# Performance work log

Hardware: AMD Instinct MI355X
Metric: run time of the kernel (lower is better)

Reference implementation:

```python
import jax, jax.numpy as jnp
import numpy as np

N = 50000      # nodes
E = 800000     # edges (avg degree 16)
IN = 128       # in_channels
H = 128        # hidden_channels
K = 20         # n_clusters
ALPHA = 0.2


def _glorot(key, shape):
    lim = float(np.sqrt(6.0 / (shape[0] + shape[1])))
    return jax.random.uniform(key, shape, jnp.float32, -lim, lim)


def setup_inputs() -> dict:
    key = jax.random.key(0)
    ks = jax.random.split(key, 12)
    x = jax.random.normal(ks[0], (N, IN), jnp.float32)
    edge_index = jax.random.randint(ks[1], (2, E), 0, N, dtype=jnp.int64)
    edge_weight = jax.random.uniform(ks[2], (E,), jnp.float32)
    perm = jax.random.permutation(ks[3], N).astype(jnp.int64)
    W1 = _glorot(ks[4], (IN, H)); b1 = jnp.zeros((H,), jnp.float32)
    W2 = _glorot(ks[5], (H, H));  b2 = jnp.zeros((H,), jnp.float32)
    W3 = _glorot(ks[6], (H, H));  b3 = jnp.zeros((H,), jnp.float32)
    W4 = _glorot(ks[7], (H, H));  b4 = jnp.zeros((H,), jnp.float32)
    prelu_a = jnp.full((H,), 0.25, jnp.float32)
    Wc = _glorot(ks[8], (H, IN)); bc = jnp.zeros((IN,), jnp.float32)
    mu = jax.random.normal(ks[9], (K, IN), jnp.float32)
    return dict(x=x, edge_index=edge_index, edge_weight=edge_weight, perm=perm,
                W1=W1, b1=b1, W2=W2, b2=b2, W3=W3, b3=b3, W4=W4, b4=b4,
                prelu_a=prelu_a, Wc=Wc, bc=bc, mu=mu)


def _gcn_norm(src, dst, ew, n):
    # add self-loops (weight 1) + symmetric normalization, PyG gcn_norm
    loop = jnp.arange(n)
    src2 = jnp.concatenate([src, loop])
    dst2 = jnp.concatenate([dst, loop])
    w2 = jnp.concatenate([ew, jnp.ones((n,), ew.dtype)])
    deg = jax.ops.segment_sum(w2, dst2, num_segments=n)
    dinv = jnp.where(deg > 0, jax.lax.rsqrt(deg), 0.0)
    norm = dinv[src2] * w2 * dinv[dst2]
    return src2, dst2, norm


def _gcn_conv(x, W, b, src2, dst2, norm, n):
    h = x @ W                              # [n, out]
    msg = h[src2] * norm[:, None]          # gather + scale
    return jax.ops.segment_sum(msg, dst2, num_segments=n) + b


def reference(x, edge_index, edge_weight, perm, W1, b1, W2, b2, W3, b3, W4, b4,
              prelu_a, Wc, bc, mu):
    n = x.shape[0]
    src, dst = edge_index[0], edge_index[1]
    src2, dst2, norm = _gcn_norm(src, dst, edge_weight, n)

    def encoder(h):
        h = _gcn_conv(h, W1, b1, src2, dst2, norm, n)
        h = _gcn_conv(h, W2, b2, src2, dst2, norm, n)
        h = _gcn_conv(h, W3, b3, src2, dst2, norm, n)
        h = _gcn_conv(h, W4, b4, src2, dst2, norm, n)
        return jnp.where(h >= 0, h, prelu_a * h)  # PReLU

    pos_z = encoder(x)
    neg_z = encoder(x[perm])                       # corruption: permute node rows
    summary = jax.nn.sigmoid(pos_z.mean(axis=0))   # [H]

    x_out = _gcn_conv(pos_z, Wc, bc, src2, dst2, norm, n)  # [N, IN]

    # Student's-t soft assignment: ||x_i - mu_k||^2 via expansion (same math)
    d = (jnp.sum(x_out * x_out, axis=1, keepdims=True)
         + jnp.sum(mu * mu, axis=1)[None, :]
         - 2.0 * (x_out @ mu.T))
    d = jnp.maximum(d, 0.0)
    q = 1.0 / (1.0 + d / ALPHA + 1e-8)
    q = q ** (ALPHA + 1.0) / 2.0
    q = q / jnp.sum(q, axis=1, keepdims=True)
    return pos_z, neg_z, summary, x_out, q
```

## Files before the change

kernel.cpp:

```cpp
#include <hip/hip_runtime.h>
#include <hip/hip_bf16.h>

constexpr int NN = 50000;
constexpr int EE = 800000;
constexpr int C  = 128;
constexpr int KC = 20;
constexpr int NB = (NN + 1023) / 1024;

typedef __attribute__((ext_vector_type(8))) short bf16x8;
typedef __attribute__((ext_vector_type(4))) float f32x4;
typedef __attribute__((ext_vector_type(4))) unsigned int u32x4;
typedef unsigned long long u64;

__device__ inline unsigned short f2bf(float f) {
    unsigned u = __float_as_uint(f);
    u += 0x7fff + ((u >> 16) & 1);
    return (unsigned short)(u >> 16);
}
__device__ inline float bf2f(unsigned short h) {
    return __uint_as_float(((unsigned)h) << 16);
}


__global__ __launch_bounds__(256) void k_scan1(const unsigned* __restrict__ cnt,
                                               unsigned* __restrict__ bsum) {
    __shared__ unsigned red[256];
    int b = blockIdx.x, t = threadIdx.x;
    int i0 = b * 1024 + t * 4;
    unsigned s = 0;
    #pragma unroll
    for (int j = 0; j < 4; ++j) { int i = i0 + j; s += (i < NN) ? cnt[i] : 0u; }
    red[t] = s; __syncthreads();
    for (int st = 128; st > 0; st >>= 1) { if (t < st) red[t] += red[t + st]; __syncthreads(); }
    if (t == 0) bsum[b] = red[0];
}

__global__ void k_scan2(unsigned* bsum, unsigned* total) {
    int t = threadIdx.x;
    unsigned v = (t < NB) ? bsum[t] : 0u;
    unsigned x = v;
    #pragma unroll
    for (int s = 1; s < 64; s <<= 1) { unsigned u = __shfl_up(x, s, 64); if (t >= s) x += u; }
    if (t < NB) bsum[t] = x - v;
    if (t == 63) *total = x;
}

__global__ __launch_bounds__(256) void k_scan3(const unsigned* __restrict__ cnt,
                                               const unsigned* __restrict__ bsum,
                                               const unsigned* __restrict__ total,
                                               unsigned* __restrict__ off,
                                               unsigned* __restrict__ cursor) {
    __shared__ unsigned wred[4];
    int b = blockIdx.x, t = threadIdx.x, lane = t & 63, wv = t >> 6;
    int i0 = b * 1024 + t * 4;
    unsigned v[4]; unsigned s = 0;
    #pragma unroll
    for (int j = 0; j < 4; ++j) { int i = i0 + j; v[j] = (i < NN) ? cnt[i] : 0u; s += v[j]; }
    unsigned x = s;
    #pragma unroll
    for (int st = 1; st < 64; st <<= 1) { unsigned u = __shfl_up(x, st, 64); if (lane >= st) x += u; }
    if (lane == 63) wred[wv] = x;
    __syncthreads();
    unsigned woff = 0;
    for (int k = 0; k < 4; ++k) if (k < wv) woff += wred[k];
    unsigned excl = bsum[b] + woff + x - s;
    #pragma unroll
    for (int j = 0; j < 4; ++j) {
        int i = i0 + j;
        if (i < NN) { off[i] = excl; cursor[i] = excl; excl += v[j]; }
    }
    if (b == 0 && t == 0) off[NN] = *total;
}

__global__ void k_fill(const int* __restrict__ ei, const float* __restrict__ ew,
                       unsigned* cursor, uint2* __restrict__ em) {
    int e = blockIdx.x * 256 + threadIdx.x;
    if (e >= EE) return;
    int s = __builtin_nontemporal_load(ei + e);
    int d = __builtin_nontemporal_load(ei + EE + e);
    float ww = __builtin_nontemporal_load(ew + e);
    unsigned p = atomicAdd(&cursor[d], 1u);
    u64 v = (u64)__float_as_uint(ww) << 32 | (unsigned)s;
    __builtin_nontemporal_store(v, (u64*)(em + p));
}

__global__ void k_dinv_csr(const unsigned* __restrict__ off,
                           const uint2* __restrict__ em, float* __restrict__ dinv) {
    int i = blockIdx.x * 256 + threadIdx.x;
    if (i >= NN) return;
    unsigned p0 = off[i], p1 = off[i + 1];
    float s = 1.0f;
    for (unsigned p = p0; p < p1; ++p) s += __uint_as_float(em[p].y);
    dinv[i] = (s > 0.f) ? rsqrtf(s) : 0.f;
}

__global__ void k_scale(const unsigned* __restrict__ off, const float* __restrict__ dinv,
                        uint2* __restrict__ em) {
    int i = blockIdx.x * 256 + threadIdx.x;
    if (i >= NN) return;
    float di = dinv[i];
    unsigned p0 = off[i], p1 = off[i + 1];
    for (unsigned p = p0; p < p1; ++p) {
        uint2 e = em[p];
        em[p].y = __float_as_uint(dinv[e.x] * __uint_as_float(e.y) * di);
    }
}


__global__ void k_wsplit(const float* W0, const float* W1, const float* W2,
                         const float* W3, const float* W4,
                         unsigned short* __restrict__ wt) {
    int m = blockIdx.x >> 6;
    const float* W = (m == 0) ? W0 : (m == 1) ? W1 : (m == 2) ? W2 : (m == 3) ? W3 : W4;
    int idx = (blockIdx.x & 63) * 256 + threadIdx.x;
    int k = idx >> 7, j = idx & 127;
    float v = W[idx];
    unsigned short h = f2bf(v);
    unsigned short* hi = wt + (size_t)(2 * m) * C * C;
    unsigned short* lo = wt + (size_t)(2 * m + 1) * C * C;
    hi[j * C + k] = h;
    lo[j * C + k] = f2bf(v - bf2f(h));
}


__global__ __launch_bounds__(256) void k_hist_mm(const int* __restrict__ ei,
                                                 unsigned* cnt,
                                                 const float* __restrict__ A,
                                                 const unsigned short* __restrict__ Bh,
                                                 const unsigned short* __restrict__ Bl,
                                                 unsigned short* __restrict__ G,
                                                 int histBlocks) {
    int tid = threadIdx.x;
    if (blockIdx.x < histBlocks) {
        int e = blockIdx.x * 256 + tid;
        if (e < EE) atomicAdd(&cnt[__builtin_nontemporal_load(ei + EE + e)], 1u);
        return;
    }
    __shared__ unsigned short Ah[64 * 128];
    __shared__ unsigned short Al[64 * 128];
    int lane = tid & 63;
    int wv   = tid >> 6;
    int row0 = (blockIdx.x - histBlocks) * 64;

    {
        int r  = tid >> 2;
        int c0 = (tid & 3) * 32;
        int gr = row0 + r;
        bool ok = gr < NN;
        const float* src = A + (size_t)(ok ? gr : 0) * C + c0;
        #pragma unroll
        for (int g = 0; g < 4; ++g) {
            float f[8];
            if (ok) {
                *(float4*)&f[0] = *(const float4*)(src + g * 8);
                *(float4*)&f[4] = *(const float4*)(src + g * 8 + 4);
            } else {
                #pragma unroll
                for (int j = 0; j < 8; ++j) f[j] = 0.f;
            }
            union { unsigned short u[8]; uint4 v; } ph, pl;
            #pragma unroll
            for (int j = 0; j < 8; ++j) {
                unsigned short h = f2bf(f[j]);
                ph.u[j] = h;
                pl.u[j] = f2bf(f[j] - bf2f(h));
            }
            int k = c0 + g * 8;
            int byte = (r * 256 + k * 2) ^ ((r & 7) << 4);
            *(uint4*)((char*)Ah + byte) = ph.v;
            *(uint4*)((char*)Al + byte) = pl.v;
        }
    }

    bf16x8 bh[2][4], bl[2][4];
    #pragma unroll
    for (int cf = 0; cf < 2; ++cf) {
        int col = wv * 32 + cf * 16 + (lane & 15);
        #pragma unroll
        for (int kt = 0; kt < 4; ++kt) {
            int k = kt * 32 + (lane >> 4) * 8;
            bh[cf][kt] = *(const bf16x8*)(Bh + (size_t)col * C + k);
            bl[cf][kt] = *(const bf16x8*)(Bl + (size_t)col * C + k);
        }
    }

    __syncthreads();

    f32x4 zero = {0.f, 0.f, 0.f, 0.f};
    f32x4 acc[4][2];
    #pragma unroll
    for (int rf = 0; rf < 4; ++rf)
        #pragma unroll
        for (int cf = 0; cf < 2; ++cf) acc[rf][cf] = zero;

    #pragma unroll
    for (int rf = 0; rf < 4; ++rf) {
        int row = rf * 16 + (lane & 15);
        #pragma unroll
        for (int kt = 0; kt < 4; ++kt) {
            int k = kt * 32 + (lane >> 4) * 8;
            int byte = (row * 256 + k * 2) ^ ((row & 7) << 4);
            bf16x8 ah = *(const bf16x8*)((const char*)Ah + byte);
            bf16x8 al = *(const bf16x8*)((const char*)Al + byte);
            #pragma unroll
            for (int cf = 0; cf < 2; ++cf) {
                acc[rf][cf] = __builtin_amdgcn_mfma_f32_16x16x32_bf16(ah, bh[cf][kt], acc[rf][cf], 0, 0, 0);
                acc[rf][cf] = __builtin_amdgcn_mfma_f32_16x16x32_bf16(al, bh[cf][kt], acc[rf][cf], 0, 0, 0);
                acc[rf][cf] = __builtin_amdgcn_mfma_f32_16x16x32_bf16(ah, bl[cf][kt], acc[rf][cf], 0, 0, 0);
            }
        }
    }

    #pragma unroll
    for (int cf = 0; cf < 2; ++cf) {
        int col = wv * 32 + cf * 16 + (lane & 15);
        #pragma unroll
        for (int rf = 0; rf < 4; ++rf) {
            #pragma unroll
            for (int q = 0; q < 4; ++q) {
                int row = row0 + rf * 16 + (lane >> 4) * 4 + q;
                if (row < NN) G[(size_t)row * C + col] = f2bf(acc[rf][cf][q]);
            }
        }
    }
}


__global__ __launch_bounds__(256) void k_mm2(const unsigned short* __restrict__ Ap,
                                             const unsigned short* __restrict__ An,
                                             const unsigned short* __restrict__ Bh,
                                             const unsigned short* __restrict__ Bl,
                                             unsigned short* __restrict__ Gp,
                                             unsigned short* __restrict__ Gn, int nblk) {
    __shared__ unsigned short Ah[64 * 128];
    int tid  = threadIdx.x;
    int lane = tid & 63;
    int wv   = tid >> 6;
    int chain = blockIdx.x >= nblk;
    int blk   = chain ? blockIdx.x - nblk : blockIdx.x;
    const unsigned short* A = chain ? An : Ap;
    unsigned short*       G = chain ? Gn : Gp;
    int row0 = blk * 64;

    {
        int r  = tid >> 2;
        int c0 = (tid & 3) * 32;
        int gr = row0 + r;
        bool ok = gr < NN;
        const unsigned short* s = A + (size_t)(ok ? gr : 0) * C + c0;
        #pragma unroll
        for (int g = 0; g < 4; ++g) {
            uint4 v = ok ? *(const uint4*)(s + g * 8) : make_uint4(0, 0, 0, 0);
            int k = c0 + g * 8;
            int byte = (r * 256 + k * 2) ^ ((r & 7) << 4);
            *(uint4*)((char*)Ah + byte) = v;
        }
    }

    bf16x8 bh[2][4], bl[2][4];
    #pragma unroll
    for (int cf = 0; cf < 2; ++cf) {
        int col = wv * 32 + cf * 16 + (lane & 15);
        #pragma unroll
        for (int kt = 0; kt < 4; ++kt) {
            int k = kt * 32 + (lane >> 4) * 8;
            bh[cf][kt] = *(const bf16x8*)(Bh + (size_t)col * C + k);
            bl[cf][kt] = *(const bf16x8*)(Bl + (size_t)col * C + k);
        }
    }

    __syncthreads();

    f32x4 zero = {0.f, 0.f, 0.f, 0.f};
    f32x4 acc[4][2];
    #pragma unroll
    for (int rf = 0; rf < 4; ++rf)
        #pragma unroll
        for (int cf = 0; cf < 2; ++cf) acc[rf][cf] = zero;

    #pragma unroll
    for (int rf = 0; rf < 4; ++rf) {
        int row = rf * 16 + (lane & 15);
        #pragma unroll
        for (int kt = 0; kt < 4; ++kt) {
            int k = kt * 32 + (lane >> 4) * 8;
            int byte = (row * 256 + k * 2) ^ ((row & 7) << 4);
            bf16x8 a = *(const bf16x8*)((const char*)Ah + byte);
            #pragma unroll
            for (int cf = 0; cf < 2; ++cf) {
                acc[rf][cf] = __builtin_amdgcn_mfma_f32_16x16x32_bf16(a, bh[cf][kt], acc[rf][cf], 0, 0, 0);
                acc[rf][cf] = __builtin_amdgcn_mfma_f32_16x16x32_bf16(a, bl[cf][kt], acc[rf][cf], 0, 0, 0);
            }
        }
    }

    #pragma unroll
    for (int cf = 0; cf < 2; ++cf) {
        int col = wv * 32 + cf * 16 + (lane & 15);
        #pragma unroll
        for (int rf = 0; rf < 4; ++rf) {
            #pragma unroll
            for (int q = 0; q < 4; ++q) {
                int row = row0 + rf * 16 + (lane >> 4) * 4 + q;
                if (row < NN) G[(size_t)row * C + col] = f2bf(acc[rf][cf][q]);
            }
        }
    }
}


__global__ __launch_bounds__(256) void k_agg2(const unsigned short* __restrict__ Gp,
                                              const unsigned short* __restrict__ Gn,
                                              const int* __restrict__ permN,
                                              const float* __restrict__ dinv,
                                              const unsigned* __restrict__ off,
                                              const uint2* __restrict__ em,
                                              const float* __restrict__ bias,
                                              const float* __restrict__ prelu,
                                              unsigned short* planeP, unsigned short* planeN,
                                              float* fP, float* fN, int nb) {
    __shared__ uint2 sem[4][64];
    int tid   = threadIdx.x;
    int chain = blockIdx.x >= nb;
    int blk   = chain ? blockIdx.x - nb : blockIdx.x;
    int lane  = tid & 63;
    int wid   = tid >> 6;
    int half  = lane >> 5;
    int gg    = (lane >> 4) & 1;
    int il    = lane & 15;
    int l32   = lane & 31;
    int i     = (blk * 4 + wid) * 2 + half;
    bool act  = i < NN;
    const unsigned short* Gsel = chain ? Gn : Gp;
    const int*            prm  = chain ? permN : nullptr;
    const uint4* H4 = (const uint4*)Gsel;

    float a[8];
    {
        int si = act ? (prm ? prm[i] : i) : 0;
        uint4 hv = H4[(size_t)si * 16 + il];
        float dv = act ? dinv[i] : 0.f;
        float sn = (gg == 0) ? dv * dv : 0.f;
        a[0] = __uint_as_float(hv.x << 16) * sn;
        a[1] = __uint_as_float(hv.x & 0xffff0000u) * sn;
        a[2] = __uint_as_float(hv.y << 16) * sn;
        a[3] = __uint_as_float(hv.y & 0xffff0000u) * sn;
        a[4] = __uint_as_float(hv.z << 16) * sn;
        a[5] = __uint_as_float(hv.z & 0xffff0000u) * sn;
        a[6] = __uint_as_float(hv.w << 16) * sn;
        a[7] = __uint_as_float(hv.w & 0xffff0000u) * sn;
    }

    unsigned p0 = 0, p1 = 0;
    if (act) { p0 = off[i]; p1 = off[i + 1]; }
    for (unsigned base = p0; base < p1; base += 32) {
        unsigned rem = p1 - base;
        int cap = rem < 32u ? (int)rem : 32;
        u64 ev = __builtin_nontemporal_load(
            (const u64*)(em + base + ((unsigned)l32 < rem ? (unsigned)l32 : 0u)));
        sem[wid][half * 32 + l32] = make_uint2((unsigned)ev, (unsigned)(ev >> 32));
        #pragma unroll 4
        for (int t = gg; t < cap; t += 2) {
            uint2 e = sem[wid][half * 32 + t];
            unsigned sv = e.x;
            if (prm) sv = (unsigned)prm[sv];
            float wv = __uint_as_float(e.y);
            uint4 hv = H4[(size_t)sv * 16 + il];
            a[0] += __uint_as_float(hv.x << 16) * wv;
            a[1] += __uint_as_float(hv.x & 0xffff0000u) * wv;
            a[2] += __uint_as_float(hv.y << 16) * wv;
            a[3] += __uint_as_float(hv.y & 0xffff0000u) * wv;
            a[4] += __uint_as_float(hv.z << 16) * wv;
            a[5] += __uint_as_float(hv.z & 0xffff0000u) * wv;
            a[6] += __uint_as_float(hv.w << 16) * wv;
            a[7] += __uint_as_float(hv.w & 0xffff0000u) * wv;
        }
    }

    #pragma unroll
    for (int j = 0; j < 8; ++j)
        a[j] += __shfl_xor(a[j], 16, 64);

    {
        float bv[8];
        *(float4*)&bv[0] = *(const float4*)(bias + il * 8);
        *(float4*)&bv[4] = *(const float4*)(bias + il * 8 + 4);
        #pragma unroll
        for (int j = 0; j < 8; ++j) a[j] += bv[j];
        if (prelu) {
            float pv[8];
            *(float4*)&pv[0] = *(const float4*)(prelu + il * 8);
            *(float4*)&pv[4] = *(const float4*)(prelu + il * 8 + 4);
            #pragma unroll
            for (int j = 0; j < 8; ++j) a[j] = (a[j] >= 0.f) ? a[j] : pv[j] * a[j];
        }
    }

    unsigned short* plane = chain ? planeN : planeP;
    float*          fo    = chain ? fN : fP;
    if (act) {
        if (gg == 0 && plane) {
            u32x4 o = { (unsigned)f2bf(a[0]) | ((unsigned)f2bf(a[1]) << 16),
                        (unsigned)f2bf(a[2]) | ((unsigned)f2bf(a[3]) << 16),
                        (unsigned)f2bf(a[4]) | ((unsigned)f2bf(a[5]) << 16),
                        (unsigned)f2bf(a[6]) | ((unsigned)f2bf(a[7]) << 16) };
            __builtin_nontemporal_store(o, (u32x4*)((uint4*)plane + (size_t)i * 16 + il));
        }
        if (fo) {
            f32x4 v0 = { a[0], a[1], a[2], a[3] };
            f32x4 v1 = { a[4], a[5], a[6], a[7] };
            if (gg == 0) __builtin_nontemporal_store(v0, (f32x4*)(fo + (size_t)i * C + il * 8));
            else         __builtin_nontemporal_store(v1, (f32x4*)(fo + (size_t)i * C + il * 8 + 4));
        }
    }
}


__global__ __launch_bounds__(256) void k_sum(const float* __restrict__ pos, float* sumbuf) {
    __shared__ float red[256];
    int t = threadIdx.x;
    int c = t & 127;
    int half = t >> 7;
    float acc = 0.f;
    for (int r = blockIdx.x * 2 + half; r < NN; r += gridDim.x * 2)
        acc += pos[(size_t)r * C + c];
    red[t] = acc;
    __syncthreads();
    if (half == 0) atomicAdd(&sumbuf[c], acc + red[t + 128]);
}

__global__ void k_summary(const float* sumbuf, float* out) {
    int t = threadIdx.x;
    if (t < C) {
        float m = sumbuf[t] * (1.0f / (float)NN);
        out[t] = 1.0f / (1.0f + expf(-m));
    }
}


__global__ __launch_bounds__(256) void k_q(const float* __restrict__ xo,
                                           const float* __restrict__ mu,
                                           float* __restrict__ qout) {
    __shared__ float sx[64][132];
    __shared__ float smu[KC][128];
    __shared__ float smun[KC];
    int tid = threadIdx.x;
    for (int idx = tid; idx < KC * 128; idx += 256)
        smu[idx >> 7][idx & 127] = mu[idx];
    __syncthreads();
    if (tid < KC) {
        float s = 0.f;
        #pragma unroll 4
        for (int j = 0; j < 128; ++j) { float m = smu[tid][j]; s += m * m; }
        smun[tid] = s;
    }
    int n0 = blockIdx.x * 64;
    for (int idx = tid; idx < 64 * 32; idx += 256) {
        int r = idx >> 5;
        int c = (idx & 31) * 4;
        int gr = n0 + r;
        float4 v = make_float4(0.f, 0.f, 0.f, 0.f);
        if (gr < NN) v = *(const float4*)(xo + (size_t)gr * C + c);
        *(float4*)&sx[r][c] = v;
    }
    __syncthreads();
    int lr = tid >> 2;
    int g  = tid & 3;
    int node = n0 + lr;
    if (node < NN) {
        float ss = 0.f;
        #pragma unroll 8
        for (int j = 0; j < 128; ++j) { float x = sx[lr][j]; ss += x * x; }
        float qv[5]; float qs = 0.f;
        #pragma unroll
        for (int kk = 0; kk < 5; ++kk) {
            int k = g * 5 + kk;
            float dot = 0.f;
            #pragma unroll 8
            for (int j = 0; j < 128; ++j) dot += sx[lr][j] * smu[k][j];
            float d = ss + smun[k] - 2.0f * dot;
            d = fmaxf(d, 0.f);
            float q = 1.0f / (1.0f + d * 5.0f + 1e-8f);
            q = powf(q, 1.2f) * 0.5f;
            qv[kk] = q; qs += q;
        }
        qs += __shfl_xor(qs, 1, 64);
        qs += __shfl_xor(qs, 2, 64);
        float inv = 1.0f / qs;
        #pragma unroll
        for (int kk = 0; kk < 5; ++kk)
            qout[(size_t)node * KC + g * 5 + kk] = qv[kk] * inv;
    }
}


extern "C" void kernel_launch(void* const* d_in, const int* in_sizes, int n_in,
                              void* d_out, int out_size, void* d_ws, size_t ws_size,
                              hipStream_t stream) {
    const float* x    = (const float*)d_in[0];
    const int*   ei   = (const int*)d_in[1];
    const float* ew   = (const float*)d_in[2];
    const int*   perm = (const int*)d_in[3];
    const float* W1 = (const float*)d_in[4];  const float* b1 = (const float*)d_in[5];
    const float* W2 = (const float*)d_in[6];  const float* b2 = (const float*)d_in[7];
    const float* W3 = (const float*)d_in[8];  const float* b3 = (const float*)d_in[9];
    const float* W4 = (const float*)d_in[10]; const float* b4 = (const float*)d_in[11];
    const float* prelu_a = (const float*)d_in[12];
    const float* Wc = (const float*)d_in[13]; const float* bc = (const float*)d_in[14];
    const float* mu = (const float*)d_in[15];

    float* out     = (float*)d_out;
    float* pos_z   = out;
    float* neg_z   = out + (size_t)NN * C;
    float* summary = out + (size_t)2 * NN * C;
    float* xout    = summary + C;
    float* qout    = xout + (size_t)NN * C;

    char* w = (char*)d_ws;
    auto carve = [&](size_t bytes) { void* p = (void*)w; w += (bytes + 511) & ~(size_t)511; return p; };
    float*          dinv   = (float*)carve((size_t)NN * 4);
    unsigned*       cnt    = (unsigned*)carve((size_t)(NN + 1) * 4);
    unsigned*       cursor = (unsigned*)carve((size_t)NN * 4);
    unsigned*       bsum   = (unsigned*)carve(256 * 4);
    unsigned*       total  = (unsigned*)carve(64);
    uint2*          em     = (uint2*)carve((size_t)EE * 8);
    float*          sumbuf = (float*)carve(512);
    unsigned short* wt     = (unsigned short*)carve((size_t)5 * 2 * C * C * 2);
    unsigned short* Gp     = (unsigned short*)carve((size_t)NN * C * 2);
    unsigned short* Gn     = (unsigned short*)carve((size_t)NN * C * 2);
    unsigned short* P0     = (unsigned short*)carve((size_t)NN * C * 2);
    unsigned short* P1     = (unsigned short*)carve((size_t)NN * C * 2);
    unsigned short* P2     = (unsigned short*)carve((size_t)NN * C * 2);

    unsigned short* Wh[5], *Wl[5];
    for (int m = 0; m < 5; ++m) {
        Wh[m] = wt + (size_t)(2 * m) * C * C;
        Wl[m] = wt + (size_t)(2 * m + 1) * C * C;
    }

    hipMemsetAsync(cnt, 0, (size_t)(NN + 1) * 4, stream);
    hipMemsetAsync(sumbuf, 0, 512, stream);

    int gE = (EE + 255) / 256, gN = (NN + 255) / 256;
    int gM = (NN + 63) / 64;
    int gA = (NN + 7) / 8;

    k_wsplit<<<320, 256, 0, stream>>>(W1, W2, W3, W4, Wc, wt);

    k_hist_mm<<<gE + gM, 256, 0, stream>>>(ei, cnt, x, Wh[0], Wl[0], Gp, gE);

    k_scan1<<<NB, 256, 0, stream>>>(cnt, bsum);
    k_scan2<<<1, 64, 0, stream>>>(bsum, total);
    k_scan3<<<NB, 256, 0, stream>>>(cnt, bsum, total, cnt, cursor);
    k_fill <<<gE, 256, 0, stream>>>(ei, ew, cursor, em);
    k_dinv_csr<<<gN, 256, 0, stream>>>(cnt, em, dinv);
    k_scale<<<gN, 256, 0, stream>>>(cnt, dinv, em);

    k_agg2<<<2 * gA, 256, 0, stream>>>(Gp, Gp, perm, dinv, cnt, em, b1, nullptr,
                                       P0, P1, nullptr, nullptr, gA);
    k_mm2 <<<2 * gM, 256, 0, stream>>>(P0, P1, Wh[1], Wl[1], Gp, Gn, gM);
    k_agg2<<<2 * gA, 256, 0, stream>>>(Gp, Gn, nullptr, dinv, cnt, em, b2, nullptr,
                                       P0, P1, nullptr, nullptr, gA);
    k_mm2 <<<2 * gM, 256, 0, stream>>>(P0, P1, Wh[2], Wl[2], Gp, Gn, gM);
    k_agg2<<<2 * gA, 256, 0, stream>>>(Gp, Gn, nullptr, dinv, cnt, em, b3, nullptr,
                                       P0, P1, nullptr, nullptr, gA);
    k_mm2 <<<2 * gM, 256, 0, stream>>>(P0, P1, Wh[3], Wl[3], Gp, Gn, gM);
    k_agg2<<<2 * gA, 256, 0, stream>>>(Gp, Gn, nullptr, dinv, cnt, em, b4, prelu_a,
                                       P2, nullptr, pos_z, neg_z, gA);
    k_mm2 <<<gM, 256, 0, stream>>>(P2, P2, Wh[4], Wl[4], Gp, Gn, gM);
    k_agg2<<<gA, 256, 0, stream>>>(Gp, Gp, nullptr, dinv, cnt, em, bc, nullptr,
                                   nullptr, nullptr, xout, nullptr, gA);

    k_sum<<<256, 256, 0, stream>>>(pos_z, sumbuf);
    k_summary<<<1, 128, 0, stream>>>(sumbuf, summary);

    k_q<<<(NN + 63) / 64, 256, 0, stream>>>(xout, mu, qout);
}
```

Baseline: 593.5 us.

## Fuse positive and negative chain aggregation into one kernel sharing edge reads

The aggregation kernel now processes the positive and corrupted chains together for the same destination node. Each CSR edge entry is loaded once and used for two gathers, instead of two separate blocks each reading the edge list. A templated flag removes the permutation lookup when it is not needed, and a specialised single-chain kernel handles the final output layer. The cost is twice the accumulator registers per thread, which may lower occupancy, and the edge-fill store is switched from nontemporal to a normal store.

```diff
diff --git a/kernel.cpp b/kernel.cpp
--- a/kernel.cpp
+++ b/kernel.cpp
@@ -80,8 +80,7 @@
     int d = __builtin_nontemporal_load(ei + EE + e);
     float ww = __builtin_nontemporal_load(ew + e);
     unsigned p = atomicAdd(&cursor[d], 1u);
-    u64 v = (u64)__float_as_uint(ww) << 32 | (unsigned)s;
-    __builtin_nontemporal_store(v, (u64*)(em + p));
+    em[p] = make_uint2((unsigned)s, __float_as_uint(ww));
 }
 
 __global__ void k_dinv_csr(const unsigned* __restrict__ off,
@@ -309,46 +308,55 @@
 }
 
 
-__global__ __launch_bounds__(256) void k_agg2(const unsigned short* __restrict__ Gp,
+template<bool PERMN>
+__global__ __launch_bounds__(256) void k_agg3(const unsigned short* __restrict__ Gp,
                                               const unsigned short* __restrict__ Gn,
-                                              const int* __restrict__ permN,
+                                              const int* __restrict__ perm,
                                               const float* __restrict__ dinv,
                                               const unsigned* __restrict__ off,
                                               const uint2* __restrict__ em,
                                               const float* __restrict__ bias,
                                               const float* __restrict__ prelu,
                                               unsigned short* planeP, unsigned short* planeN,
-                                              float* fP, float* fN, int nb) {
+                                              float* fP, float* fN) {
     __shared__ uint2 sem[4][64];
-    int tid   = threadIdx.x;
-    int chain = blockIdx.x >= nb;
-    int blk   = chain ? blockIdx.x - nb : blockIdx.x;
-    int lane  = tid & 63;
-    int wid   = tid >> 6;
-    int half  = lane >> 5;
-    int gg    = (lane >> 4) & 1;
-    int il    = lane & 15;
-    int l32   = lane & 31;
-    int i     = (blk * 4 + wid) * 2 + half;
-    bool act  = i < NN;
-    const unsigned short* Gsel = chain ? Gn : Gp;
-    const int*            prm  = chain ? permN : nullptr;
-    const uint4* H4 = (const uint4*)Gsel;
-
-    float a[8];
+    int tid  = threadIdx.x;
+    int lane = tid & 63;
+    int wid  = tid >> 6;
+    int half = lane >> 5;
+    int gg   = (lane >> 4) & 1;
+    int il   = lane & 15;
+    int l32  = lane & 31;
+    int i    = ((int)blockIdx.x * 4 + wid) * 2 + half;
+    bool act = i < NN;
+    const uint4* HP = (const uint4*)Gp;
+    const uint4* HN = (const uint4*)Gn;
+
+    float ap[8], an[8];
     {
-        int si = act ? (prm ? prm[i] : i) : 0;
-        uint4 hv = H4[(size_t)si * 16 + il];
+        int ii = act ? i : 0;
+        int sp = ii;
+        int sn_ = PERMN ? perm[ii] : ii;
+        uint4 hp = HP[(size_t)sp * 16 + il];
+        uint4 hn = HN[(size_t)sn_ * 16 + il];
         float dv = act ? dinv[i] : 0.f;
-        float sn = (gg == 0) ? dv * dv : 0.f;
-        a[0] = __uint_as_float(hv.x << 16) * sn;
-        a[1] = __uint_as_float(hv.x & 0xffff0000u) * sn;
-        a[2] = __uint_as_float(hv.y << 16) * sn;
-        a[3] = __uint_as_float(hv.y & 0xffff0000u) * sn;
-        a[4] = __uint_as_float(hv.z << 16) * sn;
-        a[5] = __uint_as_float(hv.z & 0xffff0000u) * sn;
-        a[6] = __uint_as_float(hv.w << 16) * sn;
-        a[7] = __uint_as_float(hv.w & 0xffff0000u) * sn;
+        float sc = (gg == 0) ? dv * dv : 0.f;
+        ap[0] = __uint_as_float(hp.x << 16) * sc;
+        ap[1] = __uint_as_float(hp.x & 0xffff0000u) * sc;
+        ap[2] = __uint_as_float(hp.y << 16) * sc;
+        ap[3] = __uint_as_float(hp.y & 0xffff0000u) * sc;
+        ap[4] = __uint_as_float(hp.z << 16) * sc;
+        ap[5] = __uint_as_float(hp.z & 0xffff0000u) * sc;
+        ap[6] = __uint_as_float(hp.w << 16) * sc;
+        ap[7] = __uint_as_float(hp.w & 0xffff0000u) * sc;
+        an[0] = __uint_as_float(hn.x << 16) * sc;
+        an[1] = __uint_as_float(hn.x & 0xffff0000u) * sc;
+        an[2] = __uint_as_float(hn.y << 16) * sc;
+        an[3] = __uint_as_float(hn.y & 0xffff0000u) * sc;
+        an[4] = __uint_as_float(hn.z << 16) * sc;
+        an[5] = __uint_as_float(hn.z & 0xffff0000u) * sc;
+        an[6] = __uint_as_float(hn.w << 16) * sc;
+        an[7] = __uint_as_float(hn.w & 0xffff0000u) * sc;
     }
 
     unsigned p0 = 0, p1 = 0;
@@ -362,10 +370,131 @@
         #pragma unroll 4
         for (int t = gg; t < cap; t += 2) {
             uint2 e = sem[wid][half * 32 + t];
-            unsigned sv = e.x;
-            if (prm) sv = (unsigned)prm[sv];
+            unsigned sp = e.x;
+            unsigned sn_ = PERMN ? (unsigned)perm[e.x] : e.x;
             float wv = __uint_as_float(e.y);
-            uint4 hv = H4[(size_t)sv * 16 + il];
+            uint4 hp = HP[(size_t)sp * 16 + il];
+            uint4 hn = HN[(size_t)sn_ * 16 + il];
+            ap[0] += __uint_as_float(hp.x << 16) * wv;
+            ap[1] += __uint_as_float(hp.x & 0xffff0000u) * wv;
+            ap[2] += __uint_as_float(hp.y << 16) * wv;
+            ap[3] += __uint_as_float(hp.y & 0xffff0000u) * wv;
+            ap[4] += __uint_as_float(hp.z << 16) * wv;
+            ap[5] += __uint_as_float(hp.z & 0xffff0000u) * wv;
+            ap[6] += __uint_as_float(hp.w << 16) * wv;
+            ap[7] += __uint_as_float(hp.w & 0xffff0000u) * wv;
+            an[0] += __uint_as_float(hn.x << 16) * wv;
+            an[1] += __uint_as_float(hn.x & 0xffff0000u) * wv;
+            an[2] += __uint_as_float(hn.y << 16) * wv;
+            an[3] += __uint_as_float(hn.y & 0xffff0000u) * wv;
+            an[4] += __uint_as_float(hn.z << 16) * wv;
+            an[5] += __uint_as_float(hn.z & 0xffff0000u) * wv;
+            an[6] += __uint_as_float(hn.w << 16) * wv;
+            an[7] += __uint_as_float(hn.w & 0xffff0000u) * wv;
+        }
+    }
+
+    #pragma unroll
+    for (int j = 0; j < 8; ++j) {
+        ap[j] += __shfl_xor(ap[j], 16, 64);
+        an[j] += __shfl_xor(an[j], 16, 64);
+    }
+
+    {
+        float bv[8];
+        *(float4*)&bv[0] = *(const float4*)(bias + il * 8);
+        *(float4*)&bv[4] = *(const float4*)(bias + il * 8 + 4);
+        #pragma unroll
+        for (int j = 0; j < 8; ++j) { ap[j] += bv[j]; an[j] += bv[j]; }
+        if (prelu) {
+            float pv[8];
+            *(float4*)&pv[0] = *(const float4*)(prelu + il * 8);
+            *(float4*)&pv[4] = *(const float4*)(prelu + il * 8 + 4);
+            #pragma unroll
+            for (int j = 0; j < 8; ++j) {
+                ap[j] = (ap[j] >= 0.f) ? ap[j] : pv[j] * ap[j];
+                an[j] = (an[j] >= 0.f) ? an[j] : pv[j] * an[j];
+            }
+        }
+    }
+
+    if (act) {
+        if (gg == 0 && planeP) {
+            u32x4 o = { (unsigned)f2bf(ap[0]) | ((unsigned)f2bf(ap[1]) << 16),
+                        (unsigned)f2bf(ap[2]) | ((unsigned)f2bf(ap[3]) << 16),
+                        (unsigned)f2bf(ap[4]) | ((unsigned)f2bf(ap[5]) << 16),
+                        (unsigned)f2bf(ap[6]) | ((unsigned)f2bf(ap[7]) << 16) };
+            __builtin_nontemporal_store(o, (u32x4*)((uint4*)planeP + (size_t)i * 16 + il));
+        }
+        if (gg == 1 && planeN) {
+            u32x4 o = { (unsigned)f2bf(an[0]) | ((unsigned)f2bf(an[1]) << 16),
+                        (unsigned)f2bf(an[2]) | ((unsigned)f2bf(an[3]) << 16),
+                        (unsigned)f2bf(an[4]) | ((unsigned)f2bf(an[5]) << 16),
+                        (unsigned)f2bf(an[6]) | ((unsigned)f2bf(an[7]) << 16) };
+            __builtin_nontemporal_store(o, (u32x4*)((uint4*)planeN + (size_t)i * 16 + il));
+        }
+        if (fP) {
+            f32x4 v0 = { ap[0], ap[1], ap[2], ap[3] };
+            f32x4 v1 = { ap[4], ap[5], ap[6], ap[7] };
+            if (gg == 0) __builtin_nontemporal_store(v0, (f32x4*)(fP + (size_t)i * C + il * 8));
+            else         __builtin_nontemporal_store(v1, (f32x4*)(fP + (size_t)i * C + il * 8 + 4));
+        }
+        if (fN) {
+            f32x4 v0 = { an[0], an[1], an[2], an[3] };
+            f32x4 v1 = { an[4], an[5], an[6], an[7] };
+            if (gg == 1) __builtin_nontemporal_store(v0, (f32x4*)(fN + (size_t)i * C + il * 8));
+            else         __builtin_nontemporal_store(v1, (f32x4*)(fN + (size_t)i * C + il * 8 + 4));
+        }
+    }
+}
+
+
+__global__ __launch_bounds__(256) void k_agg2(const unsigned short* __restrict__ G,
+                                              const float* __restrict__ dinv,
+                                              const unsigned* __restrict__ off,
+                                              const uint2* __restrict__ em,
+                                              const float* __restrict__ bias,
+                                              float* __restrict__ fo) {
+    __shared__ uint2 sem[4][64];
+    int tid  = threadIdx.x;
+    int lane = tid & 63;
+    int wid  = tid >> 6;
+    int half = lane >> 5;
+    int gg   = (lane >> 4) & 1;
+    int il   = lane & 15;
+    int l32  = lane & 31;
+    int i    = ((int)blockIdx.x * 4 + wid) * 2 + half;
+    bool act = i < NN;
+    const uint4* H4 = (const uint4*)G;
+
+    float a[8];
+    {
+        uint4 hv = H4[(size_t)(act ? i : 0) * 16 + il];
+        float dv = act ? dinv[i] : 0.f;
+        float sn = (gg == 0) ? dv * dv : 0.f;
+        a[0] = __uint_as_float(hv.x << 16) * sn;
+        a[1] = __uint_as_float(hv.x & 0xffff0000u) * sn;
+        a[2] = __uint_as_float(hv.y << 16) * sn;
+        a[3] = __uint_as_float(hv.y & 0xffff0000u) * sn;
+        a[4] = __uint_as_float(hv.z << 16) * sn;
+        a[5] = __uint_as_float(hv.z & 0xffff0000u) * sn;
+        a[6] = __uint_as_float(hv.w << 16) * sn;
+        a[7] = __uint_as_float(hv.w & 0xffff0000u) * sn;
+    }
+
+    unsigned p0 = 0, p1 = 0;
+    if (act) { p0 = off[i]; p1 = off[i + 1]; }
+    for (unsigned base = p0; base < p1; base += 32) {
+        unsigned rem = p1 - base;
+        int cap = rem < 32u ? (int)rem : 32;
+        u64 ev = __builtin_nontemporal_load(
+            (const u64*)(em + base + ((unsigned)l32 < rem ? (unsigned)l32 : 0u)));
+        sem[wid][half * 32 + l32] = make_uint2((unsigned)ev, (unsigned)(ev >> 32));
+        #pragma unroll 4
+        for (int t = gg; t < cap; t += 2) {
+            uint2 e = sem[wid][half * 32 + t];
+            float wv = __uint_as_float(e.y);
+            uint4 hv = H4[(size_t)e.x * 16 + il];
             a[0] += __uint_as_float(hv.x << 16) * wv;
             a[1] += __uint_as_float(hv.x & 0xffff0000u) * wv;
             a[2] += __uint_as_float(hv.y << 16) * wv;
@@ -387,31 +516,13 @@
         *(float4*)&bv[4] = *(const float4*)(bias + il * 8 + 4);
         #pragma unroll
         for (int j = 0; j < 8; ++j) a[j] += bv[j];
-        if (prelu) {
-            float pv[8];
-            *(float4*)&pv[0] = *(const float4*)(prelu + il * 8);
-            *(float4*)&pv[4] = *(const float4*)(prelu + il * 8 + 4);
-            #pragma unroll
-            for (int j = 0; j < 8; ++j) a[j] = (a[j] >= 0.f) ? a[j] : pv[j] * a[j];
-        }
-    }
-
-    unsigned short* plane = chain ? planeN : planeP;
-    float*          fo    = chain ? fN : fP;
+    }
+
     if (act) {
-        if (gg == 0 && plane) {
-            u32x4 o = { (unsigned)f2bf(a[0]) | ((unsigned)f2bf(a[1]) << 16),
-                        (unsigned)f2bf(a[2]) | ((unsigned)f2bf(a[3]) << 16),
-                        (unsigned)f2bf(a[4]) | ((unsigned)f2bf(a[5]) << 16),
-                        (unsigned)f2bf(a[6]) | ((unsigned)f2bf(a[7]) << 16) };
-            __builtin_nontemporal_store(o, (u32x4*)((uint4*)plane + (size_t)i * 16 + il));
-        }
-        if (fo) {
-            f32x4 v0 = { a[0], a[1], a[2], a[3] };
-            f32x4 v1 = { a[4], a[5], a[6], a[7] };
-            if (gg == 0) __builtin_nontemporal_store(v0, (f32x4*)(fo + (size_t)i * C + il * 8));
-            else         __builtin_nontemporal_store(v1, (f32x4*)(fo + (size_t)i * C + il * 8 + 4));
-        }
+        f32x4 v0 = { a[0], a[1], a[2], a[3] };
+        f32x4 v1 = { a[4], a[5], a[6], a[7] };
+        if (gg == 0) __builtin_nontemporal_store(v0, (f32x4*)(fo + (size_t)i * C + il * 8));
+        else         __builtin_nontemporal_store(v1, (f32x4*)(fo + (size_t)i * C + il * 8 + 4));
     }
 }
 
@@ -556,20 +667,19 @@
     k_dinv_csr<<<gN, 256, 0, stream>>>(cnt, em, dinv);
     k_scale<<<gN, 256, 0, stream>>>(cnt, dinv, em);
 
-    k_agg2<<<2 * gA, 256, 0, stream>>>(Gp, Gp, perm, dinv, cnt, em, b1, nullptr,
-                                       P0, P1, nullptr, nullptr, gA);
+    k_agg3<true><<<gA, 256, 0, stream>>>(Gp, Gp, perm, dinv, cnt, em, b1, nullptr,
+                                         P0, P1, nullptr, nullptr);
     k_mm2 <<<2 * gM, 256, 0, stream>>>(P0, P1, Wh[1], Wl[1], Gp, Gn, gM);
-    k_agg2<<<2 * gA, 256, 0, stream>>>(Gp, Gn, nullptr, dinv, cnt, em, b2, nullptr,
-                                       P0, P1, nullptr, nullptr, gA);
+    k_agg3<false><<<gA, 256, 0, stream>>>(Gp, Gn, nullptr, dinv, cnt, em, b2, nullptr,
+                                          P0, P1, nullptr, nullptr);
     k_mm2 <<<2 * gM, 256, 0, stream>>>(P0, P1, Wh[2], Wl[2], Gp, Gn, gM);
-    k_agg2<<<2 * gA, 256, 0, stream>>>(Gp, Gn, nullptr, dinv, cnt, em, b3, nullptr,
-                                       P0, P1, nullptr, nullptr, gA);
+    k_agg3<false><<<gA, 256, 0, stream>>>(Gp, Gn, nullptr, dinv, cnt, em, b3, nullptr,
+                                          P0, P1, nullptr, nullptr);
     k_mm2 <<<2 * gM, 256, 0, stream>>>(P0, P1, Wh[3], Wl[3], Gp, Gn, gM);
-    k_agg2<<<2 * gA, 256, 0, stream>>>(Gp, Gn, nullptr, dinv, cnt, em, b4, prelu_a,
-                                       P2, nullptr, pos_z, neg_z, gA);
+    k_agg3<false><<<gA, 256, 0, stream>>>(Gp, Gn, nullptr, dinv, cnt, em, b4, prelu_a,
+                                          P2, nullptr, pos_z, neg_z);
     k_mm2 <<<gM, 256, 0, stream>>>(P2, P2, Wh[4], Wl[4], Gp, Gn, gM);
-    k_agg2<<<gA, 256, 0, stream>>>(Gp, Gp, nullptr, dinv, cnt, em, bc, nullptr,
-                                   nullptr, nullptr, xout, nullptr, gA);
+    k_agg2<<<gA, 256, 0, stream>>>(Gp, dinv, cnt, em, bc, xout);
 
     k_sum<<<256, 256, 0, stream>>>(pos_z, sumbuf);
     k_summary<<<1, 128, 0, stream>>>(sumbuf, summary);
```

After: 586.9 us. About the same (-1.1%).
